# Optimization experiments

Measured on AMD Instinct MI355X. Metric: run time of the kernel, lower is better.

Reference implementation:

```python
import jax, jax.numpy as jnp
import numpy as np

H, C = 4, 32          # heads, per-head channels (hidden=128)
NEG_SLOPE = 0.2        # PyG GATv2Conv default LeakyReLU slope


def setup_inputs() -> dict:
    key = jax.random.key(0)
    ks = jax.random.split(key, 9)
    N_a, N_m = 100000, 50000     # asset / market node counts
    E_aa, E_am = 600000, 400000  # edge counts per edge type
    D, L = 128, 2                # hidden dims, num GAT layers
    sc = 1.0 / np.sqrt(D).astype(np.float32)

    x_asset = jax.random.normal(ks[0], (N_a, D), jnp.float32)
    x_market = jax.random.normal(ks[1], (N_m, D), jnp.float32)

    edge_aa = jax.random.randint(ks[2], (2, E_aa), 0, N_a, jnp.int32)
    src_am = jax.random.randint(ks[3], (E_am,), 0, N_a, jnp.int32)
    dst_am = jax.random.randint(ks[4], (E_am,), 0, N_m, jnp.int32)
    edge_am = jnp.stack([src_am, dst_am])

    Wl = jax.random.normal(ks[5], (L, D, D), jnp.float32) * sc   # lin_l (src)
    Wr = jax.random.normal(ks[6], (L, D, D), jnp.float32) * sc   # lin_r (dst)
    att = jax.random.normal(ks[7], (L, H, C), jnp.float32) * sc  # attention vector
    bias = jnp.zeros((L, D), jnp.float32)

    return {"x_asset": x_asset, "x_market": x_market,
            "edge_aa": edge_aa, "edge_am": edge_am,
            "Wl": Wl, "Wr": Wr, "att": att, "bias": bias}


def _gatv2(x_src, x_dst, src, dst, Wl, Wr, att, bias):
    """One GATv2Conv: gather-attend-scatter. x_src:[Ns,D], x_dst:[Nd,D]."""
    N_dst = x_dst.shape[0]
    xl = (x_src @ Wl).reshape(-1, H, C)   # transformed src (messages)
    xr = (x_dst @ Wr).reshape(-1, H, C)   # transformed dst
    z = jax.nn.leaky_relu(xl[src] + xr[dst], NEG_SLOPE)     # [E,H,C]
    e = jnp.einsum('ehc,hc->eh', z, att)                    # [E,H] scores
    # softmax over incoming edges per destination node
    m = jax.lax.stop_gradient(jax.ops.segment_max(e, dst, num_segments=N_dst))
    w = jnp.exp(e - m[dst])
    s = jax.ops.segment_sum(w, dst, num_segments=N_dst)
    alpha = w / jnp.maximum(s[dst], jnp.float32(1e-16))     # [E,H]
    out = jax.ops.segment_sum(alpha[..., None] * xl[src], dst, num_segments=N_dst)
    return out.reshape(N_dst, H * C) + bias


def reference(x_asset, x_market, edge_aa, edge_am, Wl, Wr, att, bias):
    # Faithful to source: x_dict is never updated between layers, so every
    # layer reads the ORIGINAL features and only the last layer's dict is kept.
    L = Wl.shape[0]
    out_asset = out_market = None
    for l in range(L):
        out_asset = _gatv2(x_asset, x_asset, edge_aa[0], edge_aa[1],
                           Wl[l], Wr[l], att[l], bias[l])
        out_market = _gatv2(x_asset, x_market, edge_am[0], edge_am[1],
                            Wl[l], Wr[l], att[l], bias[l])
    return out_asset, out_market
```

## Files before the change

kernel.cpp:

```cpp
#include <hip/hip_runtime.h>
#include <hip/hip_bf16.h>


#define NEG_SLOPE 0.2f

typedef __attribute__((ext_vector_type(8))) short short8;
typedef __attribute__((ext_vector_type(4))) float floatx4;

__device__ inline unsigned short f2bf(float x) {
    union { float f; unsigned u; } v; v.f = x;
    unsigned r = v.u + 0x7FFF + ((v.u >> 16) & 1);
    return (unsigned short)(r >> 16);
}
__device__ inline float bf2f(unsigned short h) {
    union { unsigned u; float f; } v; v.u = (unsigned)h << 16;
    return v.f;
}

__global__ __launch_bounds__(512) void gemm_mfma(const float* __restrict__ X,
                                                 const float* __restrict__ W,
                                                 float* __restrict__ C, int M) {
    __shared__ __align__(16) unsigned char lds[65536];

    const int t = threadIdx.x;
    {
        const int n = t & 127;
        const int kh = t >> 7;
        unsigned short hb[32], lb[32];
#pragma unroll
        for (int i = 0; i < 32; ++i) {
            int k = kh * 32 + i;
            float w = W[(size_t)k * 128 + n];
            unsigned short h = f2bf(w);
            hb[i] = h;
            lb[i] = f2bf(w - bf2f(h));
        }
#pragma unroll
        for (int j = 0; j < 4; ++j) {
            int k = kh * 32 + j * 8;
            int off = ((n * 256 + k * 2) ^ ((n & 7) << 4));
            short8 hv, lv;
#pragma unroll
            for (int i = 0; i < 8; ++i) { hv[i] = (short)hb[j * 8 + i]; lv[i] = (short)lb[j * 8 + i]; }
            *(short8*)(&lds[off]) = hv;
            *(short8*)(&lds[32768 + off]) = lv;
        }
    }
    __syncthreads();

    const int wv = t >> 6;
    const int l = t & 63;
    const int lr = l & 15;
    const int lkb = (l >> 4) * 8;
    const int arow = blockIdx.x * 128 + wv * 16 + lr;

    short8 ah[4], al[4];
    if (arow < M) {
#pragma unroll
        for (int ks = 0; ks < 4; ++ks) {
            const float* xp = X + (size_t)arow * 128 + ks * 32 + lkb;
            float4 f0 = *(const float4*)xp;
            float4 f1 = *(const float4*)(xp + 4);
            float xv[8] = {f0.x, f0.y, f0.z, f0.w, f1.x, f1.y, f1.z, f1.w};
            short8 h, lo;
#pragma unroll
            for (int i = 0; i < 8; ++i) {
                unsigned short hb = f2bf(xv[i]);
                h[i] = (short)hb;
                lo[i] = (short)f2bf(xv[i] - bf2f(hb));
            }
            ah[ks] = h; al[ks] = lo;
        }
    } else {
#pragma unroll
        for (int ks = 0; ks < 4; ++ks) { ah[ks] = (short8)0; al[ks] = (short8)0; }
    }

    floatx4 acc[8];
#pragma unroll
    for (int ct = 0; ct < 8; ++ct) acc[ct] = (floatx4)0.f;

#pragma unroll
    for (int ks = 0; ks < 4; ++ks) {
#pragma unroll
        for (int ct = 0; ct < 8; ++ct) {
            int n = ct * 16 + lr;
            int off = ((n * 256 + (ks * 32 + lkb) * 2) ^ ((n & 7) << 4));
            short8 bh = *(const short8*)(&lds[off]);
            short8 bl = *(const short8*)(&lds[32768 + off]);
            acc[ct] = __builtin_amdgcn_mfma_f32_16x16x32_bf16(ah[ks], bh, acc[ct], 0, 0, 0);
            acc[ct] = __builtin_amdgcn_mfma_f32_16x16x32_bf16(al[ks], bh, acc[ct], 0, 0, 0);
            acc[ct] = __builtin_amdgcn_mfma_f32_16x16x32_bf16(ah[ks], bl, acc[ct], 0, 0, 0);
        }
    }

    const int orow0 = blockIdx.x * 128 + wv * 16 + (l >> 4) * 4;
#pragma unroll
    for (int ct = 0; ct < 8; ++ct) {
        int col = ct * 16 + lr;
#pragma unroll
        for (int r = 0; r < 4; ++r) {
            int orow = orow0 + r;
            if (orow < M) C[(size_t)orow * 128 + col] = acc[ct][r];
        }
    }
}

__global__ void degcount(const int* __restrict__ aadst, const int* __restrict__ amdst,
                         int* __restrict__ deg, int Eaa, int Eam, int Na) {
    int i = blockIdx.x * 256 + threadIdx.x;
    if (i < Eaa) atomicAdd(&deg[aadst[i]], 1);
    else if (i < Eaa + Eam) atomicAdd(&deg[Na + amdst[i - Eaa]], 1);
}

__global__ void scan_bsum(const int* __restrict__ deg, int* __restrict__ bsum, int N) {
    __shared__ int sd[256];
    int t = threadIdx.x;
    int base = blockIdx.x * 1024 + t * 4;
    int s = 0;
#pragma unroll
    for (int q = 0; q < 4; ++q) { int idx = base + q; if (idx < N) s += deg[idx]; }
    sd[t] = s; __syncthreads();
    for (int off = 128; off > 0; off >>= 1) {
        if (t < off) sd[t] += sd[t + off];
        __syncthreads();
    }
    if (t == 0) bsum[blockIdx.x] = sd[0];
}

__global__ void scan_partials(int* __restrict__ bsum, int nblk) {
    __shared__ int sd[256];
    int t = threadIdx.x;
    int v = (t < nblk) ? bsum[t] : 0;
    sd[t] = v; __syncthreads();
    for (int off = 1; off < 256; off <<= 1) {
        int x = sd[t];
        if (t >= off) x += sd[t - off];
        __syncthreads(); sd[t] = x; __syncthreads();
    }
    if (t < nblk) bsum[t] = (t == 0) ? 0 : sd[t - 1];
    if (t == 0) bsum[nblk] = sd[255];
}

__global__ void scan_final(const int* __restrict__ deg, const int* __restrict__ bsum,
                           int* __restrict__ row_start, int* __restrict__ fill,
                           int N, int nblk) {
    __shared__ int sd[256];
    int t = threadIdx.x;
    int base = blockIdx.x * 1024 + t * 4;
    int v[4]; int s = 0;
#pragma unroll
    for (int q = 0; q < 4; ++q) { int idx = base + q; v[q] = (idx < N) ? deg[idx] : 0; s += v[q]; }
    sd[t] = s; __syncthreads();
    for (int off = 1; off < 256; off <<= 1) {
        int x = sd[t];
        if (t >= off) x += sd[t - off];
        __syncthreads(); sd[t] = x; __syncthreads();
    }
    int run = bsum[blockIdx.x] + ((t == 0) ? 0 : sd[t - 1]);
#pragma unroll
    for (int q = 0; q < 4; ++q) {
        int idx = base + q;
        if (idx < N) { row_start[idx] = run; fill[idx] = run; }
        run += v[q];
    }
    if (blockIdx.x == 0 && t == 0) row_start[N] = bsum[nblk];
}

__global__ void fillcsr(const int* __restrict__ aasrc, const int* __restrict__ aadst,
                        const int* __restrict__ amsrc, const int* __restrict__ amdst,
                        int* __restrict__ fill, int* __restrict__ csr,
                        int Eaa, int Eam, int Na) {
    int i = blockIdx.x * 256 + threadIdx.x;
    int src, d;
    if (i < Eaa) { src = aasrc[i]; d = aadst[i]; }
    else if (i < Eaa + Eam) { src = amsrc[i - Eaa]; d = Na + amdst[i - Eaa]; }
    else return;
    int pos = atomicAdd(&fill[d], 1);
    csr[pos] = src;
}

__global__ __launch_bounds__(256) void gather_gat(const float* __restrict__ XLa,
                                                  const int* __restrict__ csr,
                                                  const int* __restrict__ row_start,
                                                  const float* __restrict__ att,
                                                  const float* __restrict__ bias,
                                                  float* __restrict__ out,
                                                  int Ntot) {
    int wid = (blockIdx.x * 256 + threadIdx.x) >> 6;
    int lane = threadIdx.x & 63;
    if (wid >= Ntot) return;
    const int h = lane >> 4;

    const float2 av = *(const float2*)(att + h * 32 + (lane & 15) * 2);
    const float2 xr = *(const float2*)(out + (size_t)wid * 128 + lane * 2);

    int j = row_start[wid];
    const int end = row_start[wid + 1];
    float s = 0.f;
    float2 acc = make_float2(0.f, 0.f);

#define SCORE(xl, p)                                                     \
    {                                                                    \
        float z0 = xl.x + xr.x; z0 = (z0 > 0.f) ? z0 : NEG_SLOPE * z0;   \
        float z1 = xl.y + xr.y; z1 = (z1 > 0.f) ? z1 : NEG_SLOPE * z1;   \
        p = z0 * av.x + z1 * av.y;                                       \
    }

    for (; j + 4 <= end; j += 4) {
        int s0 = csr[j], s1 = csr[j + 1], s2 = csr[j + 2], s3 = csr[j + 3];
        float2 x0 = *(const float2*)(XLa + (size_t)s0 * 128 + lane * 2);
        float2 x1 = *(const float2*)(XLa + (size_t)s1 * 128 + lane * 2);
        float2 x2 = *(const float2*)(XLa + (size_t)s2 * 128 + lane * 2);
        float2 x3 = *(const float2*)(XLa + (size_t)s3 * 128 + lane * 2);
        float p0, p1, p2, p3;
        SCORE(x0, p0); SCORE(x1, p1); SCORE(x2, p2); SCORE(x3, p3);
        p0 += __shfl_xor(p0, 1);  p1 += __shfl_xor(p1, 1);
        p2 += __shfl_xor(p2, 1);  p3 += __shfl_xor(p3, 1);
        p0 += __shfl_xor(p0, 2);  p1 += __shfl_xor(p1, 2);
        p2 += __shfl_xor(p2, 2);  p3 += __shfl_xor(p3, 2);
        p0 += __shfl_xor(p0, 4);  p1 += __shfl_xor(p1, 4);
        p2 += __shfl_xor(p2, 4);  p3 += __shfl_xor(p3, 4);
        p0 += __shfl_xor(p0, 8);  p1 += __shfl_xor(p1, 8);
        p2 += __shfl_xor(p2, 8);  p3 += __shfl_xor(p3, 8);
        float w0 = __expf(p0), w1 = __expf(p1), w2 = __expf(p2), w3 = __expf(p3);
        s += (w0 + w1) + (w2 + w3);
        acc.x += (w0 * x0.x + w1 * x1.x) + (w2 * x2.x + w3 * x3.x);
        acc.y += (w0 * x0.y + w1 * x1.y) + (w2 * x2.y + w3 * x3.y);
    }
    for (; j < end; ++j) {
        int src = csr[j];
        float2 xl = *(const float2*)(XLa + (size_t)src * 128 + lane * 2);
        float p;
        SCORE(xl, p);
        p += __shfl_xor(p, 1);
        p += __shfl_xor(p, 2);
        p += __shfl_xor(p, 4);
        p += __shfl_xor(p, 8);
        float w = __expf(p);
        s += w;
        acc.x += w * xl.x;
        acc.y += w * xl.y;
    }
#undef SCORE

    float inv = 1.f / fmaxf(s, 1e-16f);
    const float2 bv = *(const float2*)(bias + lane * 2);
    float2 o = make_float2(acc.x * inv + bv.x, acc.y * inv + bv.y);
    *(float2*)(out + (size_t)wid * 128 + lane * 2) = o;
}

extern "C" void kernel_launch(void* const* d_in, const int* in_sizes, int n_in,
                              void* d_out, int out_size, void* d_ws, size_t ws_size,
                              hipStream_t stream) {
    const float* x_asset  = (const float*)d_in[0];
    const float* x_market = (const float*)d_in[1];
    const int*   eaa      = (const int*)d_in[2];
    const int*   eam      = (const int*)d_in[3];
    const float* Wl       = (const float*)d_in[4];
    const float* Wr       = (const float*)d_in[5];
    const float* att      = (const float*)d_in[6];
    const float* bias     = (const float*)d_in[7];

    const int Na  = in_sizes[0] / 128;
    const int Nm  = in_sizes[1] / 128;
    const int Eaa = in_sizes[2] / 2;
    const int Eam = in_sizes[3] / 2;
    const int Ntot = Na + Nm;
    const int E = Eaa + Eam;

    const float* Wl1   = Wl + 128 * 128;
    const float* Wr1   = Wr + 128 * 128;
    const float* att1  = att + 128;
    const float* bias1 = bias + 128;

    float* XLa = (float*)d_ws;
    int*   deg = (int*)(XLa + (size_t)Na * 128);
    int*   fill = deg + Ntot;
    int*   bsum = fill + Ntot;
    int*   row_start = bsum + 260;
    int*   csr = row_start + Ntot + 1;

    float* XR = (float*)d_out;

    hipMemsetAsync(deg, 0, sizeof(int) * (size_t)Ntot, stream);

    gemm_mfma<<<(Na + 127) / 128, 512, 0, stream>>>(x_asset, Wl1, XLa, Na);
    gemm_mfma<<<(Na + 127) / 128, 512, 0, stream>>>(x_asset, Wr1, XR, Na);
    gemm_mfma<<<(Nm + 127) / 128, 512, 0, stream>>>(x_market, Wr1, XR + (size_t)Na * 128, Nm);

    degcount<<<(E + 255) / 256, 256, 0, stream>>>(eaa + Eaa, eam + Eam, deg, Eaa, Eam, Na);

    const int nblk = (Ntot + 1023) / 1024;
    scan_bsum<<<nblk, 256, 0, stream>>>(deg, bsum, Ntot);
    scan_partials<<<1, 256, 0, stream>>>(bsum, nblk);
    scan_final<<<nblk, 256, 0, stream>>>(deg, bsum, row_start, fill, Ntot, nblk);

    fillcsr<<<(E + 255) / 256, 256, 0, stream>>>(eaa, eaa + Eaa, eam, eam + Eam,
                                                 fill, csr, Eaa, Eam, Na);

    gather_gat<<<(Ntot * 64 + 255) / 256, 256, 0, stream>>>(
        XLa, csr, row_start, att1, bias1, (float*)d_out, Ntot);
}
```

Measured before the change: 405.1 us.

## Fuse asset GEMMs, vectorize edge kernels, process two edges per wave in gather

The two asset-side GEMMs are merged into one kernel that converts the X tile once and stages each weight matrix in turn, which avoids re-reading and re-splitting x_asset. Degree counting and CSR fill now read edge indices as int4, so each thread handles four edges. The gather kernel splits the wave into two halves that each process a different edge with float4 loads, and combines the halves at the end with a cross-half shuffle. This trades extra per-edge masking and a final reduction for fewer loop iterations and wider memory accesses.

```diff
diff --git a/kernel.cpp b/kernel.cpp
--- a/kernel.cpp
+++ b/kernel.cpp
@@ -17,37 +17,38 @@
     return v.f;
 }
 
-__global__ __launch_bounds__(512) void gemm_mfma(const float* __restrict__ X,
-                                                 const float* __restrict__ W,
-                                                 float* __restrict__ C, int M) {
+__device__ inline void stage_w(const float* __restrict__ W, unsigned char* lds, int t) {
+    const int n = t & 127;
+    const int kh = t >> 7;
+    unsigned short hb[32], lb[32];
+#pragma unroll
+    for (int i = 0; i < 32; ++i) {
+        int k = kh * 32 + i;
+        float w = W[(size_t)k * 128 + n];
+        unsigned short h = f2bf(w);
+        hb[i] = h;
+        lb[i] = f2bf(w - bf2f(h));
+    }
+#pragma unroll
+    for (int j = 0; j < 4; ++j) {
+        int k = kh * 32 + j * 8;
+        int off = ((n * 256 + k * 2) ^ ((n & 7) << 4));
+        short8 hv, lv;
+#pragma unroll
+        for (int i = 0; i < 8; ++i) { hv[i] = (short)hb[j * 8 + i]; lv[i] = (short)lb[j * 8 + i]; }
+        *(short8*)(&lds[off]) = hv;
+        *(short8*)(&lds[32768 + off]) = lv;
+    }
+}
+
+__global__ __launch_bounds__(512) void gemm_asset(const float* __restrict__ X,
+                                                  const float* __restrict__ W1,
+                                                  const float* __restrict__ W2,
+                                                  float* __restrict__ C1,
+                                                  float* __restrict__ C2, int M) {
     __shared__ __align__(16) unsigned char lds[65536];
 
     const int t = threadIdx.x;
-    {
-        const int n = t & 127;
-        const int kh = t >> 7;
-        unsigned short hb[32], lb[32];
-#pragma unroll
-        for (int i = 0; i < 32; ++i) {
-            int k = kh * 32 + i;
-            float w = W[(size_t)k * 128 + n];
-            unsigned short h = f2bf(w);
-            hb[i] = h;
-            lb[i] = f2bf(w - bf2f(h));
-        }
-#pragma unroll
-        for (int j = 0; j < 4; ++j) {
-            int k = kh * 32 + j * 8;
-            int off = ((n * 256 + k * 2) ^ ((n & 7) << 4));
-            short8 hv, lv;
-#pragma unroll
-            for (int i = 0; i < 8; ++i) { hv[i] = (short)hb[j * 8 + i]; lv[i] = (short)lb[j * 8 + i]; }
-            *(short8*)(&lds[off]) = hv;
-            *(short8*)(&lds[32768 + off]) = lv;
-        }
-    }
-    __syncthreads();
-
     const int wv = t >> 6;
     const int l = t & 63;
     const int lr = l & 15;
@@ -76,10 +77,82 @@
         for (int ks = 0; ks < 4; ++ks) { ah[ks] = (short8)0; al[ks] = (short8)0; }
     }
 
+    const int orow0 = blockIdx.x * 128 + wv * 16 + (l >> 4) * 4;
+
+#pragma unroll
+    for (int ph = 0; ph < 2; ++ph) {
+        if (ph) __syncthreads();
+        stage_w(ph ? W2 : W1, lds, t);
+        __syncthreads();
+        float* __restrict__ C = ph ? C2 : C1;
+
+        floatx4 acc[8];
+#pragma unroll
+        for (int ct = 0; ct < 8; ++ct) acc[ct] = (floatx4)0.f;
+#pragma unroll
+        for (int ks = 0; ks < 4; ++ks) {
+#pragma unroll
+            for (int ct = 0; ct < 8; ++ct) {
+                int n = ct * 16 + lr;
+                int off = ((n * 256 + (ks * 32 + lkb) * 2) ^ ((n & 7) << 4));
+                short8 bh = *(const short8*)(&lds[off]);
+                short8 bl = *(const short8*)(&lds[32768 + off]);
+                acc[ct] = __builtin_amdgcn_mfma_f32_16x16x32_bf16(ah[ks], bh, acc[ct], 0, 0, 0);
+                acc[ct] = __builtin_amdgcn_mfma_f32_16x16x32_bf16(al[ks], bh, acc[ct], 0, 0, 0);
+                acc[ct] = __builtin_amdgcn_mfma_f32_16x16x32_bf16(ah[ks], bl, acc[ct], 0, 0, 0);
+            }
+        }
+#pragma unroll
+        for (int ct = 0; ct < 8; ++ct) {
+            int col = ct * 16 + lr;
+#pragma unroll
+            for (int r = 0; r < 4; ++r) {
+                int orow = orow0 + r;
+                if (orow < M) C[(size_t)orow * 128 + col] = acc[ct][r];
+            }
+        }
+    }
+}
+
+__global__ __launch_bounds__(512) void gemm_mfma(const float* __restrict__ X,
+                                                 const float* __restrict__ W,
+                                                 float* __restrict__ C, int M) {
+    __shared__ __align__(16) unsigned char lds[65536];
+    const int t = threadIdx.x;
+    stage_w(W, lds, t);
+    __syncthreads();
+
+    const int wv = t >> 6;
+    const int l = t & 63;
+    const int lr = l & 15;
+    const int lkb = (l >> 4) * 8;
+    const int arow = blockIdx.x * 128 + wv * 16 + lr;
+
+    short8 ah[4], al[4];
+    if (arow < M) {
+#pragma unroll
+        for (int ks = 0; ks < 4; ++ks) {
+            const float* xp = X + (size_t)arow * 128 + ks * 32 + lkb;
+            float4 f0 = *(const float4*)xp;
+            float4 f1 = *(const float4*)(xp + 4);
+            float xv[8] = {f0.x, f0.y, f0.z, f0.w, f1.x, f1.y, f1.z, f1.w};
+            short8 h, lo;
+#pragma unroll
+            for (int i = 0; i < 8; ++i) {
+                unsigned short hb = f2bf(xv[i]);
+                h[i] = (short)hb;
+                lo[i] = (short)f2bf(xv[i] - bf2f(hb));
+            }
+            ah[ks] = h; al[ks] = lo;
+        }
+    } else {
+#pragma unroll
+        for (int ks = 0; ks < 4; ++ks) { ah[ks] = (short8)0; al[ks] = (short8)0; }
+    }
+
     floatx4 acc[8];
 #pragma unroll
     for (int ct = 0; ct < 8; ++ct) acc[ct] = (floatx4)0.f;
-
 #pragma unroll
     for (int ks = 0; ks < 4; ++ks) {
 #pragma unroll
@@ -108,9 +181,22 @@
 
 __global__ void degcount(const int* __restrict__ aadst, const int* __restrict__ amdst,
                          int* __restrict__ deg, int Eaa, int Eam, int Na) {
+    const int nqaa = Eaa >> 2, nqam = Eam >> 2;
     int i = blockIdx.x * 256 + threadIdx.x;
-    if (i < Eaa) atomicAdd(&deg[aadst[i]], 1);
-    else if (i < Eaa + Eam) atomicAdd(&deg[Na + amdst[i - Eaa]], 1);
+    if (i < nqaa) {
+        int4 d = ((const int4*)aadst)[i];
+        atomicAdd(&deg[d.x], 1); atomicAdd(&deg[d.y], 1);
+        atomicAdd(&deg[d.z], 1); atomicAdd(&deg[d.w], 1);
+    } else if (i < nqaa + nqam) {
+        int4 d = ((const int4*)amdst)[i - nqaa];
+        atomicAdd(&deg[Na + d.x], 1); atomicAdd(&deg[Na + d.y], 1);
+        atomicAdd(&deg[Na + d.z], 1); atomicAdd(&deg[Na + d.w], 1);
+    } else {
+        int k = i - (nqaa + nqam);
+        int remaa = Eaa & 3, remam = Eam & 3;
+        if (k < remaa) atomicAdd(&deg[aadst[nqaa * 4 + k]], 1);
+        else if (k - remaa < remam) atomicAdd(&deg[Na + amdst[nqam * 4 + k - remaa]], 1);
+    }
 }
 
 __global__ void scan_bsum(const int* __restrict__ deg, int* __restrict__ bsum, int N) {
@@ -171,13 +257,30 @@
                         const int* __restrict__ amsrc, const int* __restrict__ amdst,
                         int* __restrict__ fill, int* __restrict__ csr,
                         int Eaa, int Eam, int Na) {
+    const int nqaa = Eaa >> 2, nqam = Eam >> 2;
     int i = blockIdx.x * 256 + threadIdx.x;
-    int src, d;
-    if (i < Eaa) { src = aasrc[i]; d = aadst[i]; }
-    else if (i < Eaa + Eam) { src = amsrc[i - Eaa]; d = Na + amdst[i - Eaa]; }
-    else return;
-    int pos = atomicAdd(&fill[d], 1);
-    csr[pos] = src;
+    if (i < nqaa) {
+        int4 sv = ((const int4*)aasrc)[i];
+        int4 dv = ((const int4*)aadst)[i];
+        csr[atomicAdd(&fill[dv.x], 1)] = sv.x;
+        csr[atomicAdd(&fill[dv.y], 1)] = sv.y;
+        csr[atomicAdd(&fill[dv.z], 1)] = sv.z;
+        csr[atomicAdd(&fill[dv.w], 1)] = sv.w;
+    } else if (i < nqaa + nqam) {
+        int4 sv = ((const int4*)amsrc)[i - nqaa];
+        int4 dv = ((const int4*)amdst)[i - nqaa];
+        csr[atomicAdd(&fill[Na + dv.x], 1)] = sv.x;
+        csr[atomicAdd(&fill[Na + dv.y], 1)] = sv.y;
+        csr[atomicAdd(&fill[Na + dv.z], 1)] = sv.z;
+        csr[atomicAdd(&fill[Na + dv.w], 1)] = sv.w;
+    } else {
+        int k = i - (nqaa + nqam);
+        int remaa = Eaa & 3, remam = Eam & 3;
+        if (k < remaa)
+            csr[atomicAdd(&fill[aadst[nqaa * 4 + k]], 1)] = aasrc[nqaa * 4 + k];
+        else if (k - remaa < remam)
+            csr[atomicAdd(&fill[Na + amdst[nqam * 4 + k - remaa]], 1)] = amsrc[nqam * 4 + k - remaa];
+    }
 }
 
 __global__ __launch_bounds__(256) void gather_gat(const float* __restrict__ XLa,
@@ -188,66 +291,56 @@
                                                   float* __restrict__ out,
                                                   int Ntot) {
     int wid = (blockIdx.x * 256 + threadIdx.x) >> 6;
-    int lane = threadIdx.x & 63;
+    const int l = threadIdx.x & 63;
     if (wid >= Ntot) return;
-    const int h = lane >> 4;
-
-    const float2 av = *(const float2*)(att + h * 32 + (lane & 15) * 2);
-    const float2 xr = *(const float2*)(out + (size_t)wid * 128 + lane * 2);
-
-    int j = row_start[wid];
+    const int half = l >> 5;
+    const int q = l & 31;
+
+    const float4 av = *(const float4*)(att + (q >> 3) * 32 + (q & 7) * 4);
+    const float4 xr = *(const float4*)(out + (size_t)wid * 128 + q * 4);
+
+    const int beg = row_start[wid];
     const int end = row_start[wid + 1];
     float s = 0.f;
-    float2 acc = make_float2(0.f, 0.f);
-
-#define SCORE(xl, p)                                                     \
-    {                                                                    \
-        float z0 = xl.x + xr.x; z0 = (z0 > 0.f) ? z0 : NEG_SLOPE * z0;   \
-        float z1 = xl.y + xr.y; z1 = (z1 > 0.f) ? z1 : NEG_SLOPE * z1;   \
-        p = z0 * av.x + z1 * av.y;                                       \
-    }
-
-    for (; j + 4 <= end; j += 4) {
-        int s0 = csr[j], s1 = csr[j + 1], s2 = csr[j + 2], s3 = csr[j + 3];
-        float2 x0 = *(const float2*)(XLa + (size_t)s0 * 128 + lane * 2);
-        float2 x1 = *(const float2*)(XLa + (size_t)s1 * 128 + lane * 2);
-        float2 x2 = *(const float2*)(XLa + (size_t)s2 * 128 + lane * 2);
-        float2 x3 = *(const float2*)(XLa + (size_t)s3 * 128 + lane * 2);
-        float p0, p1, p2, p3;
-        SCORE(x0, p0); SCORE(x1, p1); SCORE(x2, p2); SCORE(x3, p3);
-        p0 += __shfl_xor(p0, 1);  p1 += __shfl_xor(p1, 1);
-        p2 += __shfl_xor(p2, 1);  p3 += __shfl_xor(p3, 1);
-        p0 += __shfl_xor(p0, 2);  p1 += __shfl_xor(p1, 2);
-        p2 += __shfl_xor(p2, 2);  p3 += __shfl_xor(p3, 2);
-        p0 += __shfl_xor(p0, 4);  p1 += __shfl_xor(p1, 4);
-        p2 += __shfl_xor(p2, 4);  p3 += __shfl_xor(p3, 4);
-        p0 += __shfl_xor(p0, 8);  p1 += __shfl_xor(p1, 8);
-        p2 += __shfl_xor(p2, 8);  p3 += __shfl_xor(p3, 8);
-        float w0 = __expf(p0), w1 = __expf(p1), w2 = __expf(p2), w3 = __expf(p3);
-        s += (w0 + w1) + (w2 + w3);
-        acc.x += (w0 * x0.x + w1 * x1.x) + (w2 * x2.x + w3 * x3.x);
-        acc.y += (w0 * x0.y + w1 * x1.y) + (w2 * x2.y + w3 * x3.y);
-    }
-    for (; j < end; ++j) {
-        int src = csr[j];
-        float2 xl = *(const float2*)(XLa + (size_t)src * 128 + lane * 2);
-        float p;
-        SCORE(xl, p);
+    float4 acc = make_float4(0.f, 0.f, 0.f, 0.f);
+
+#pragma unroll 2
+    for (int j = beg; j < end; j += 2) {
+        int e = j + half;
+        bool act = (e < end);
+        int src = csr[act ? e : beg];
+        const float4 xl = *(const float4*)(XLa + (size_t)src * 128 + q * 4);
+        float z0 = xl.x + xr.x; z0 = fmaxf(z0, NEG_SLOPE * z0);
+        float z1 = xl.y + xr.y; z1 = fmaxf(z1, NEG_SLOPE * z1);
+        float z2 = xl.z + xr.z; z2 = fmaxf(z2, NEG_SLOPE * z2);
+        float z3 = xl.w + xr.w; z3 = fmaxf(z3, NEG_SLOPE * z3);
+        float p = z0 * av.x;
+        p = fmaf(z1, av.y, p);
+        p = fmaf(z2, av.z, p);
+        p = fmaf(z3, av.w, p);
         p += __shfl_xor(p, 1);
         p += __shfl_xor(p, 2);
         p += __shfl_xor(p, 4);
-        p += __shfl_xor(p, 8);
-        float w = __expf(p);
+        float w = act ? __expf(p) : 0.f;
         s += w;
-        acc.x += w * xl.x;
-        acc.y += w * xl.y;
-    }
-#undef SCORE
-
-    float inv = 1.f / fmaxf(s, 1e-16f);
-    const float2 bv = *(const float2*)(bias + lane * 2);
-    float2 o = make_float2(acc.x * inv + bv.x, acc.y * inv + bv.y);
-    *(float2*)(out + (size_t)wid * 128 + lane * 2) = o;
+        acc.x = fmaf(w, xl.x, acc.x);
+        acc.y = fmaf(w, xl.y, acc.y);
+        acc.z = fmaf(w, xl.z, acc.z);
+        acc.w = fmaf(w, xl.w, acc.w);
+    }
+    s += __shfl_xor(s, 32);
+    acc.x += __shfl_xor(acc.x, 32);
+    acc.y += __shfl_xor(acc.y, 32);
+    acc.z += __shfl_xor(acc.z, 32);
+    acc.w += __shfl_xor(acc.w, 32);
+
+    if (half == 0) {
+        float inv = 1.f / fmaxf(s, 1e-16f);
+        const float4 bv = *(const float4*)(bias + q * 4);
+        float4 o = make_float4(fmaf(acc.x, inv, bv.x), fmaf(acc.y, inv, bv.y),
+                               fmaf(acc.z, inv, bv.z), fmaf(acc.w, inv, bv.w));
+        *(float4*)(out + (size_t)wid * 128 + q * 4) = o;
+    }
 }
 
 extern "C" void kernel_launch(void* const* d_in, const int* in_sizes, int n_in,
@@ -285,19 +378,19 @@
 
     hipMemsetAsync(deg, 0, sizeof(int) * (size_t)Ntot, stream);
 
-    gemm_mfma<<<(Na + 127) / 128, 512, 0, stream>>>(x_asset, Wl1, XLa, Na);
-    gemm_mfma<<<(Na + 127) / 128, 512, 0, stream>>>(x_asset, Wr1, XR, Na);
+    gemm_asset<<<(Na + 127) / 128, 512, 0, stream>>>(x_asset, Wl1, Wr1, XLa, XR, Na);
     gemm_mfma<<<(Nm + 127) / 128, 512, 0, stream>>>(x_market, Wr1, XR + (size_t)Na * 128, Nm);
 
-    degcount<<<(E + 255) / 256, 256, 0, stream>>>(eaa + Eaa, eam + Eam, deg, Eaa, Eam, Na);
+    const int nq = (Eaa >> 2) + (Eam >> 2) + 8;
+    degcount<<<(nq + 255) / 256, 256, 0, stream>>>(eaa + Eaa, eam + Eam, deg, Eaa, Eam, Na);
 
     const int nblk = (Ntot + 1023) / 1024;
     scan_bsum<<<nblk, 256, 0, stream>>>(deg, bsum, Ntot);
     scan_partials<<<1, 256, 0, stream>>>(bsum, nblk);
     scan_final<<<nblk, 256, 0, stream>>>(deg, bsum, row_start, fill, Ntot, nblk);
 
-    fillcsr<<<(E + 255) / 256, 256, 0, stream>>>(eaa, eaa + Eaa, eam, eam + Eam,
-                                                 fill, csr, Eaa, Eam, Na);
+    fillcsr<<<(nq + 255) / 256, 256, 0, stream>>>(eaa, eaa + Eaa, eam, eam + Eam,
+                                                  fill, csr, Eaa, Eam, Na);
 
     gather_gat<<<(Ntot * 64 + 255) / 256, 256, 0, stream>>>(
         XLa, csr, row_start, att1, bias1, (float*)d_out, Ntot);
```

Measured after the change: 403.5 us. No clear change (-0.4%).
